# Kernel tuning notes

Hardware: AMD Instinct MI355X
Metric: run time of the kernel (lower is better)

## Reference

```python
import jax, jax.numpy as jnp
import numpy as np

B, S, HIDDEN, N_HEADS = 1, 2048, 2048, 16
HEAD_DIM = HIDDEN // N_HEADS  # 128


def setup_inputs() -> dict:
    key = jax.random.key(0)
    ks = jax.random.split(key, 7)
    w = 0.02  # init scale for projection weights
    return {
        "x_self": jax.random.normal(ks[0], (B, S, HIDDEN), jnp.float32),
        "x_cross": jax.random.normal(ks[1], (B, S, HIDDEN), jnp.float32),
        "mask": jnp.zeros((B, 1, S, S), jnp.float32),
        "Wq": jax.random.normal(ks[2], (HIDDEN, HIDDEN), jnp.float32) * w,
        "Wk": jax.random.normal(ks[3], (HIDDEN, HIDDEN), jnp.float32) * w,
        "Wv": jax.random.normal(ks[4], (HIDDEN, HIDDEN), jnp.float32) * w,
        "Wo": jax.random.normal(ks[5], (HIDDEN, HIDDEN), jnp.float32) * w,
    }


def reference(x_self, x_cross, mask, Wq, Wk, Wv, Wo):
    bf16 = jnp.bfloat16
    b = x_self.shape[0]
    scale = HEAD_DIM ** -0.5

    def split_heads(x):  # [b, s, hidden] -> [b, h, s, d]
        return x.reshape(b, -1, N_HEADS, HEAD_DIM).transpose(0, 2, 1, 3)

    # projections run in bf16 (weights cast to bf16 in the original)
    q_self = split_heads((x_self.astype(bf16) @ Wq.astype(bf16).T))
    q_cross = split_heads((x_cross.astype(bf16) @ Wq.astype(bf16).T))
    # k/v for both self and cross blocks come from x_self with identical weights
    k = split_heads((x_self.astype(bf16) @ Wk.astype(bf16).T))
    v = split_heads((x_self.astype(bf16) @ Wv.astype(bf16).T))

    def attn_block(qh):
        # fp32 upcast for QK^T + softmax, then bf16 cast for AV (dropout p=0 -> identity)
        w = jnp.einsum('bhqd,bhkd->bhqk', qh.astype(jnp.float32), k.astype(jnp.float32)) * scale
        w = w + mask
        w = jax.nn.softmax(w, axis=-1).astype(bf16)
        return jnp.einsum('bhqk,bhkd->bhqd', w, v.astype(bf16))  # [b, h, s, d] bf16

    out_self = attn_block(q_self)
    out_cross = attn_block(q_cross)
    out = jnp.concatenate([out_self, out_cross], axis=1)          # [b, 2h, s, d]
    out_flat = out.transpose(0, 2, 1, 3).reshape(b, -1, HIDDEN)   # [b, 2s, hidden]
    Wo_bf = Wo.astype(bf16)
    out_final = 0.5 * (out_flat @ Wo_bf.T + out_flat @ Wo_bf.T)
    return out_final.astype(jnp.float32)
```

## Files before the change

### kernel.cpp

```cpp
#include <hip/hip_runtime.h>
#include <hip/hip_bf16.h>
#include <stdint.h>

#define S 2048
#define HID 2048
#define NH 16
#define HD 128

typedef short short8 __attribute__((ext_vector_type(8)));
typedef float f32x4 __attribute__((ext_vector_type(4)));
typedef float f32x16 __attribute__((ext_vector_type(16)));
typedef uint32_t u32;
typedef u32 u32x4 __attribute__((ext_vector_type(4)));

__device__ __forceinline__ ushort f2bf(float x) {
  uint32_t u = __builtin_bit_cast(uint32_t, x);
  if ((u & 0x7fffffffu) > 0x7f800000u) return (ushort)((u >> 16) | 0x40);
  uint32_t r = u + 0x7fffu + ((u >> 16) & 1u);
  return (ushort)(r >> 16);
}
__device__ __forceinline__ float bf2f(ushort u) {
  union { uint32_t i; float f; } c; c.i = ((uint32_t)u) << 16; return c.f;
}

__device__ __forceinline__ void glds16(const ushort* g, ushort* l) {
  __builtin_amdgcn_global_load_lds((const __attribute__((address_space(1))) uint32_t*)g,
                                   (__attribute__((address_space(3))) uint32_t*)l, 16, 0, 0);
}

__device__ __forceinline__ void mfma16(f32x4& d, short8 a, short8 b) {
  asm volatile("v_mfma_f32_16x16x32_bf16 %0, %1, %2, %0" : "+v"(d) : "v"(a), "v"(b));
}
__device__ __forceinline__ void mfma32(f32x16& d, short8 a, short8 b) {
  asm volatile("v_mfma_f32_32x32x16_bf16 %0, %1, %2, %0" : "+v"(d) : "v"(a), "v"(b));
}
#define MFMA_FENCE() do {                              \
    asm volatile("s_nop 7\n\ts_nop 7\n\ts_nop 7");     \
    __builtin_amdgcn_sched_barrier(0);                 \
  } while (0)
__device__ __forceinline__ void plswap(u32& a, u32& b) {
  asm volatile("v_permlane32_swap_b32 %0, %1" : "+v"(a), "+v"(b));
}
__device__ __forceinline__ u32 cvtpk(float lo, float hi) {
  u32 r; asm volatile("v_cvt_pk_bf16_f32 %0, %1, %2" : "=v"(r) : "v"(lo), "v"(hi)); return r;
}

struct CastArgs { const float* s[6]; ushort* d[6]; };
__global__ __launch_bounds__(256) void cast6_k(CastArgs a) {
  const float* in = a.s[blockIdx.y];
  ushort* out = a.d[blockIdx.y];
  int i = blockIdx.x * 256 + threadIdx.x;
  float4 v = ((const float4*)in)[i];
  ushort4 o;
  o.x = f2bf(v.x); o.y = f2bf(v.y); o.z = f2bf(v.z); o.w = f2bf(v.w);
  ((ushort4*)out)[i] = o;
}

template <int OUTF32, int NSPLIT>
__global__ __launch_bounds__(256)
void gemm_bt_k(const ushort* __restrict__ A, const ushort* __restrict__ B,
               void* __restrict__ C, int M, int N, int K) {
  __shared__ __align__(16) ushort ldsA[128 * 64];
  __shared__ __align__(16) ushort ldsB[128 * 64];
  const int tid = threadIdx.x, lane = tid & 63, wid = tid >> 6;
  const int g = lane >> 4, c = lane & 15;
  const int wr = wid >> 1, wc = wid & 1;
  const long m0 = (long)blockIdx.y * 128, n0 = (long)blockIdx.x * 128;
  const int srow = lane >> 3, sslot = lane & 7;

  f32x4 acc[4][4] = {};

  for (int k0 = 0; k0 < K; k0 += 64) {
#pragma unroll
    for (int i = 0; i < 4; ++i) {
      int ii = wid * 4 + i;
      int rt = ii * 8 + srow;
      int col = ((sslot ^ (rt & 7)) << 3) + k0;
      glds16(A + (m0 + rt) * (long)K + col, ldsA + ii * 512);
      glds16(B + (n0 + rt) * (long)K + col, ldsB + ii * 512);
    }
    __syncthreads();
#pragma unroll
    for (int kk = 0; kk < 2; ++kk) {
      short8 af[4], bfr[4];
#pragma unroll
      for (int m = 0; m < 4; ++m) {
        int row = wr * 64 + m * 16 + c;
        af[m] = *(const short8*)(ldsA + row * 64 + (((kk * 4 + g) ^ (row & 7)) << 3));
      }
#pragma unroll
      for (int n = 0; n < 4; ++n) {
        int row = wc * 64 + n * 16 + c;
        bfr[n] = *(const short8*)(ldsB + row * 64 + (((kk * 4 + g) ^ (row & 7)) << 3));
      }
#pragma unroll
      for (int m = 0; m < 4; ++m)
#pragma unroll
        for (int n = 0; n < 4; ++n) mfma16(acc[m][n], af[m], bfr[n]);
    }
    __syncthreads();
  }
  MFMA_FENCE();
#pragma unroll
  for (int m = 0; m < 4; ++m) {
#pragma unroll
    for (int r = 0; r < 4; ++r) {
      long grow = m0 + wr * 64 + m * 16 + g * 4 + r;
#pragma unroll
      for (int n = 0; n < 4; ++n) {
        long gcol = n0 + wc * 64 + n * 16 + c;
        long idx;
        if (NSPLIT) idx = ((gcol >> 11) << 22) + (grow << 11) + (gcol & 2047);
        else        idx = grow * N + gcol;
        float v = acc[m][n][r];
        if (OUTF32) ((float*)C)[idx] = bf2f(f2bf(v));
        else        ((ushort*)C)[idx] = f2bf(v);
      }
    }
  }
}

__global__ __launch_bounds__(256)
void transpose_bf16_k(const ushort* __restrict__ in, ushort* __restrict__ out) {
  __shared__ __align__(16) ushort t[64][72];
  const int tid = threadIdx.x;
  const long bx = (long)blockIdx.x * 64;
  const long by = (long)blockIdx.y * 64;
#pragma unroll
  for (int i = 0; i < 2; ++i) {
    int row = (tid >> 3) + i * 32;
    int col = (tid & 7) * 8;
    *(short8*)(&t[row][col]) = *(const short8*)(in + (by + row) * 2048 + bx + col);
  }
  __syncthreads();
#pragma unroll
  for (int i = 0; i < 2; ++i) {
    int orow = (tid >> 3) + i * 32;
    int ocol = (tid & 7) * 8;
    short8 v;
#pragma unroll
    for (int j = 0; j < 8; ++j) v[j] = (short)t[ocol + j][orow];
    *(short8*)(out + (bx + orow) * 2048 + by + ocol) = v;
  }
}

__global__ __launch_bounds__(256)
void maskT_k(const float* __restrict__ in, ushort* __restrict__ out) {
  __shared__ ushort t[64][72];
  const int tid = threadIdx.x;
  const long q0 = (long)blockIdx.y * 64;
  const long k0 = (long)blockIdx.x * 64;
#pragma unroll
  for (int i = 0; i < 4; ++i) {
    int row = i * 16 + (tid >> 4);
    int col = (tid & 15) * 4;
    float4 v = *(const float4*)(in + (q0 + row) * S + k0 + col);
    t[col + 0][row] = f2bf(v.x);
    t[col + 1][row] = f2bf(v.y);
    t[col + 2][row] = f2bf(v.z);
    t[col + 3][row] = f2bf(v.w);
  }
  __syncthreads();
#pragma unroll
  for (int i = 0; i < 2; ++i) {
    int row = i * 32 + (tid >> 3);
    int col = (tid & 7) * 8;
    *(short8*)(out + (k0 + row) * S + q0 + col) = *(const short8*)(&t[row][col]);
  }
}

__global__ __launch_bounds__(256)
void attn4_k(const ushort* __restrict__ Qself, const ushort* __restrict__ Qcross,
             const ushort* __restrict__ Kp, const ushort* __restrict__ Vt,
             const ushort* __restrict__ maskT, ushort* __restrict__ outf) {
  __shared__ __align__(16) ushort ldsK[2 * 64 * 128];
  __shared__ __align__(16) ushort ldsV[2 * 128 * 64];
  const int tid = threadIdx.x, lane = tid & 63, wid = tid >> 6;
  const int c31 = lane & 31, hi = lane >> 5;

  const int b = blockIdx.x;
  const int xcd = b & 7, j = b >> 3;
  const int h = xcd + 8 * (j & 1);
  const int blk = (j >> 1) & 1;
  const int qt = j >> 2;

  const ushort* Qp = blk ? Qcross : Qself;
  const int qbase = qt * 128 + wid * 32;
  const long qme = qbase + c31;

  short8 qf[8];
#pragma unroll
  for (int ks = 0; ks < 8; ++ks)
    qf[ks] = *(const short8*)(Qp + qme * HID + h * HD + ks * 16 + hi * 8);

  f32x16 o[4] = {};
  float m_r = -__builtin_inff(), l_r = 0.f;

  const float SC  = 0.08838834764831845f;
  const float L2E = 1.4426950408889634f;
  const float THR = 5.545177444479562f;

  const int kRow4 = lane >> 4, kSlot = lane & 15;
  const int vRow8 = lane >> 3, vSlot = lane & 7;
  const ushort* mT = maskT + qme;

#define STAGE(BO, KV0) do {                                                       \
    _Pragma("unroll")                                                             \
    for (int i_ = 0; i_ < 4; ++i_) {                                              \
      int seg = i_ * 4 + wid;                                                     \
      int rk = seg * 4 + kRow4;                                                   \
      glds16(Kp + (long)((KV0) + rk) * HID + h * HD + ((kSlot ^ (rk & 15)) << 3), \
             ldsK + (BO) * 8192 + seg * 512);                                     \
      int rv = seg * 8 + vRow8;                                                   \
      glds16(Vt + (long)(h * HD + rv) * S + (KV0) + ((vSlot ^ (rv & 7)) << 3),    \
             ldsV + (BO) * 8192 + seg * 512);                                     \
    }                                                                             \
  } while (0)

  STAGE(0, 0);
  __syncthreads();

  for (int t = 0; t < 32; ++t) {
    const int bo = t & 1;
    const ushort* kb = ldsK + bo * 8192;
    const ushort* vb = ldsV + bo * 8192;
    if (t < 31) STAGE(bo ^ 1, (t + 1) * 64);
    const int kv0 = t * 64;

    ushort mvu0[16], mvu1[16];
#pragma unroll
    for (int r = 0; r < 16; ++r) {
      int krow = (r & 3) + 8 * (r >> 2) + 4 * hi;
      mvu0[r] = mT[(long)(kv0 + krow) * S];
      mvu1[r] = mT[(long)(kv0 + 32 + krow) * S];
    }

    f32x16 s0 = {}, s1 = {};
    __builtin_amdgcn_s_setprio(1);
#pragma unroll
    for (int ks = 0; ks < 8; ++ks) {
      int r0 = c31, r1 = 32 + c31;
      short8 kf0 = *(const short8*)(kb + r0 * 128 + (((ks * 2 + hi) ^ (r0 & 15)) << 3));
      short8 kf1 = *(const short8*)(kb + r1 * 128 + (((ks * 2 + hi) ^ (r1 & 15)) << 3));
      mfma32(s0, kf0, qf[ks]);
      mfma32(s1, kf1, qf[ks]);
    }
    __builtin_amdgcn_s_setprio(0);
    MFMA_FENCE();

#pragma unroll
    for (int r = 0; r < 16; ++r) {
      s0[r] = __builtin_fmaf(s0[r], SC, bf2f(mvu0[r]));
      s1[r] = __builtin_fmaf(s1[r], SC, bf2f(mvu1[r]));
    }

    float mx[16];
#pragma unroll
    for (int r = 0; r < 16; ++r) mx[r] = fmaxf(s0[r], s1[r]);
#pragma unroll
    for (int st = 8; st >= 1; st >>= 1)
#pragma unroll
      for (int i = 0; i < 8; ++i)
        if (i < st) mx[i] = fmaxf(mx[i], mx[i + st]);
    float pmax = fmaxf(mx[0], __shfl_xor(mx[0], 32));

    if (!__all(pmax <= m_r + THR)) {
      float mnew = fmaxf(m_r, pmax);
      float alpha = __builtin_amdgcn_exp2f((m_r - mnew) * L2E);
      m_r = mnew;
      l_r *= alpha;
#pragma unroll
      for (int r = 0; r < 16; ++r) {
        float alf = __shfl(alpha, (r & 3) + 8 * (r >> 2) + 4 * hi);
#pragma unroll
        for (int dt = 0; dt < 4; ++dt) o[dt][r] *= alf;
      }
    }

    const float nm = -m_r * L2E;
#pragma unroll
    for (int r = 0; r < 16; ++r) {
      s0[r] = __builtin_amdgcn_exp2f(__builtin_fmaf(s0[r], L2E, nm));
      s1[r] = __builtin_amdgcn_exp2f(__builtin_fmaf(s1[r], L2E, nm));
    }
    float sm[16];
#pragma unroll
    for (int r = 0; r < 16; ++r) sm[r] = s0[r] + s1[r];
#pragma unroll
    for (int st = 8; st >= 1; st >>= 1)
#pragma unroll
      for (int i = 0; i < 8; ++i)
        if (i < st) sm[i] += sm[i + st];
    l_r += sm[0] + __shfl_xor(sm[0], 32);

    short8 pa[4];
#pragma unroll
    for (int kk = 0; kk < 4; ++kk) {
      const f32x16& sv = (kk < 2) ? s0 : s1;
      const int bq = (kk & 1) * 8;
      u32 x0 = cvtpk(sv[bq + 0], sv[bq + 1]);
      u32 x1 = cvtpk(sv[bq + 2], sv[bq + 3]);
      u32 y0 = cvtpk(sv[bq + 4], sv[bq + 5]);
      u32 y1 = cvtpk(sv[bq + 6], sv[bq + 7]);
      plswap(x0, y0);
      plswap(x1, y1);
      u32x4 tt; tt[0] = x0; tt[1] = x1; tt[2] = y0; tt[3] = y1;
      pa[kk] = __builtin_bit_cast(short8, tt);
    }
    asm volatile("s_nop 1");
    __builtin_amdgcn_sched_barrier(0);

    __builtin_amdgcn_s_setprio(1);
#pragma unroll
    for (int dt = 0; dt < 4; ++dt) {
      int row = dt * 32 + c31;
#pragma unroll
      for (int kk = 0; kk < 4; ++kk) {
        short8 vf = *(const short8*)(vb + row * 64 + (((kk * 2 + hi) ^ (row & 7)) << 3));
        mfma32(o[dt], pa[kk], vf);
      }
    }
    __builtin_amdgcn_s_setprio(0);

    __syncthreads();
  }
#undef STAGE

  MFMA_FENCE();
#pragma unroll
  for (int r = 0; r < 16; ++r) {
    int qr = (r & 3) + 8 * (r >> 2) + 4 * hi;
    float linv = 1.0f / __shfl(l_r, qr);
    long orow = 2L * (qbase + qr) + blk;
#pragma unroll
    for (int dt = 0; dt < 4; ++dt)
      outf[orow * HID + h * HD + dt * 32 + c31] = f2bf(o[dt][r] * linv);
  }
}

extern "C" void kernel_launch(void* const* d_in, const int* in_sizes, int n_in,
                              void* d_out, int out_size, void* d_ws, size_t ws_size,
                              hipStream_t stream) {
  (void)in_sizes; (void)n_in; (void)out_size; (void)ws_size;
  const float* x_self  = (const float*)d_in[0];
  const float* x_cross = (const float*)d_in[1];
  const float* mask    = (const float*)d_in[2];
  const float* Wq      = (const float*)d_in[3];
  const float* Wk      = (const float*)d_in[4];
  const float* Wv      = (const float*)d_in[5];
  const float* Wo      = (const float*)d_in[6];

  uint8_t* w = (uint8_t*)d_ws;
  const size_t MB8 = (size_t)S * HID * sizeof(ushort);
  ushort* xs_bf   = (ushort*)(w + 0 * MB8);
  ushort* xc_bf   = (ushort*)(w + 1 * MB8);
  ushort* Wq_bf   = (ushort*)(w + 2 * MB8);
  ushort* Wk_bf   = (ushort*)(w + 3 * MB8);
  ushort* Wv_bf   = (ushort*)(w + 4 * MB8);
  ushort* Wo_bf   = (ushort*)(w + 5 * MB8);
  ushort* q_self  = (ushort*)(w + 6 * MB8);
  ushort* q_cross = (ushort*)(w + 7 * MB8);
  ushort* k_      = (ushort*)(w + 8 * MB8);
  ushort* v_      = (ushort*)(w + 9 * MB8);
  ushort* vt       = xs_bf;
  ushort* out_flat = Wq_bf;
  ushort* maskT    = v_;

  CastArgs ca;
  ca.s[0] = x_self;  ca.d[0] = xs_bf;
  ca.s[1] = x_cross; ca.d[1] = xc_bf;
  ca.s[2] = Wq;      ca.d[2] = Wq_bf;
  ca.s[3] = Wk;      ca.d[3] = Wk_bf;
  ca.s[4] = Wv;      ca.d[4] = Wv_bf;
  ca.s[5] = Wo;      ca.d[5] = Wo_bf;
  cast6_k<<<dim3(4096, 6), 256, 0, stream>>>(ca);

  gemm_bt_k<0, 0><<<dim3(16, 32), 256, 0, stream>>>(xs_bf, Wq_bf, q_self, 4096, 2048, 2048);
  gemm_bt_k<0, 1><<<dim3(32, 16), 256, 0, stream>>>(xs_bf, Wk_bf, k_, 2048, 4096, 2048);

  transpose_bf16_k<<<dim3(32, 32), 256, 0, stream>>>(v_, vt);
  maskT_k<<<dim3(32, 32), 256, 0, stream>>>(mask, maskT);

  attn4_k<<<dim3(512), 256, 0, stream>>>(q_self, q_cross, k_, vt, maskT, out_flat);

  gemm_bt_k<1, 0><<<dim3(16, 32), 256, 0, stream>>>(out_flat, Wo_bf, d_out, 4096, 2048, 2048);
}
```

Baseline: 253.4 us.

## Software-pipeline attention: overlap next tile's QK^T MFMAs with current softmax

The attention kernel now uses 32-row KV tiles in place of 64-row ones and restructures the loop so the QK^T MFMA cluster for tile t+1 is issued before the softmax and PV work for tile t. Two score accumulators ping-pong between iterations, and K is staged two tiles ahead while V is staged one tile ahead. The goal is to hide the exp/max/sum VALU work behind matrix-core work and to halve LDS use. The cost is twice as many iterations and barriers, and more live registers.

```diff
diff --git a/kernel.cpp b/kernel.cpp
--- a/kernel.cpp
+++ b/kernel.cpp
@@ -170,11 +170,11 @@
 }
 
 __global__ __launch_bounds__(256)
-void attn4_k(const ushort* __restrict__ Qself, const ushort* __restrict__ Qcross,
+void attn5_k(const ushort* __restrict__ Qself, const ushort* __restrict__ Qcross,
              const ushort* __restrict__ Kp, const ushort* __restrict__ Vt,
              const ushort* __restrict__ maskT, ushort* __restrict__ outf) {
-  __shared__ __align__(16) ushort ldsK[2 * 64 * 128];
-  __shared__ __align__(16) ushort ldsV[2 * 128 * 64];
+  __shared__ __align__(16) ushort ldsK[2 * 32 * 128];
+  __shared__ __align__(16) ushort ldsV[2 * 128 * 32];
   const int tid = threadIdx.x, lane = tid & 63, wid = tid >> 6;
   const int c31 = lane & 31, hi = lane >> 5;
 
@@ -194,137 +194,145 @@
     qf[ks] = *(const short8*)(Qp + qme * HID + h * HD + ks * 16 + hi * 8);
 
   f32x16 o[4] = {};
+  f32x16 sA, sB;
   float m_r = -__builtin_inff(), l_r = 0.f;
 
   const float SC  = 0.08838834764831845f;
   const float L2E = 1.4426950408889634f;
   const float THR = 5.545177444479562f;
 
-  const int kRow4 = lane >> 4, kSlot = lane & 15;
-  const int vRow8 = lane >> 3, vSlot = lane & 7;
+  const int kRow16 = lane >> 4, kSlot16 = lane & 15;
+  const int vRow4  = lane >> 2, vSlot4  = lane & 3;
   const ushort* mT = maskT + qme;
 
-#define STAGE(BO, KV0) do {                                                       \
-    _Pragma("unroll")                                                             \
-    for (int i_ = 0; i_ < 4; ++i_) {                                              \
-      int seg = i_ * 4 + wid;                                                     \
-      int rk = seg * 4 + kRow4;                                                   \
-      glds16(Kp + (long)((KV0) + rk) * HID + h * HD + ((kSlot ^ (rk & 15)) << 3), \
-             ldsK + (BO) * 8192 + seg * 512);                                     \
-      int rv = seg * 8 + vRow8;                                                   \
-      glds16(Vt + (long)(h * HD + rv) * S + (KV0) + ((vSlot ^ (rv & 7)) << 3),    \
-             ldsV + (BO) * 8192 + seg * 512);                                     \
-    }                                                                             \
+#define STAGE_K(BO, KV0) do {                                                      \
+    _Pragma("unroll")                                                              \
+    for (int i_ = 0; i_ < 2; ++i_) {                                               \
+      int seg = i_ * 4 + wid;                                                      \
+      int rk = seg * 4 + kRow16;                                                   \
+      glds16(Kp + (long)((KV0) + rk) * HID + h * HD + ((kSlot16 ^ (rk & 15)) << 3),\
+             ldsK + (BO) * 4096 + seg * 512);                                      \
+    } } while (0)
+
+#define STAGE_V(BO, KV0) do {                                                      \
+    _Pragma("unroll")                                                              \
+    for (int i_ = 0; i_ < 2; ++i_) {                                               \
+      int seg = i_ * 4 + wid;                                                      \
+      int rv = seg * 16 + vRow4;                                                   \
+      glds16(Vt + (long)(h * HD + rv) * S + (KV0) + ((vSlot4 ^ (rv & 3)) << 3),    \
+             ldsV + (BO) * 4096 + seg * 512);                                      \
+    } } while (0)
+
+#define QCLUSTER(SWR, KBASE) do {                                                  \
+    const ushort* kb_ = (KBASE);                                                   \
+    _Pragma("unroll")                                                              \
+    for (int r_ = 0; r_ < 16; ++r_) (SWR)[r_] = 0.f;                               \
+    __builtin_amdgcn_s_setprio(1);                                                 \
+    _Pragma("unroll")                                                              \
+    for (int ks = 0; ks < 8; ++ks) {                                               \
+      short8 kf = *(const short8*)(kb_ + c31 * 128 + (((ks * 2 + hi) ^ (c31 & 15)) << 3)); \
+      mfma32((SWR), kf, qf[ks]);                                                   \
+    }                                                                              \
+    __builtin_amdgcn_s_setprio(0);                                                 \
   } while (0)
 
-  STAGE(0, 0);
+#define BODY(T, SRD, SWR) do {                                                     \
+    const int kv0_ = (T) * 32;                                                     \
+    ushort mvu[16];                                                                \
+    _Pragma("unroll")                                                              \
+    for (int r = 0; r < 16; ++r) {                                                 \
+      int krow = (r & 3) + 8 * (r >> 2) + 4 * hi;                                  \
+      mvu[r] = mT[(long)(kv0_ + krow) * S];                                        \
+    }                                                                              \
+    if ((T) + 2 < 64) STAGE_K((T) & 1, ((T) + 2) * 32);                            \
+    if ((T) + 1 < 64) {                                                            \
+      STAGE_V(((T) + 1) & 1, ((T) + 1) * 32);                                      \
+      QCLUSTER(SWR, ldsK + (((T) + 1) & 1) * 4096);                                \
+    }                                                                              \
+    __builtin_amdgcn_sched_barrier(0);                                             \
+    _Pragma("unroll")                                                              \
+    for (int r = 0; r < 16; ++r)                                                   \
+      (SRD)[r] = __builtin_fmaf((SRD)[r], SC, bf2f(mvu[r]));                       \
+    float mx[8];                                                                   \
+    _Pragma("unroll")                                                              \
+    for (int i = 0; i < 8; ++i) mx[i] = fmaxf((SRD)[i], (SRD)[i + 8]);             \
+    _Pragma("unroll")                                                              \
+    for (int st = 4; st >= 1; st >>= 1)                                            \
+      _Pragma("unroll")                                                            \
+      for (int i = 0; i < 4; ++i)                                                  \
+        if (i < st) mx[i] = fmaxf(mx[i], mx[i + st]);                              \
+    float pmax = fmaxf(mx[0], __shfl_xor(mx[0], 32));                              \
+    if (!__all(pmax <= m_r + THR)) {                                               \
+      float mnew = fmaxf(m_r, pmax);                                               \
+      float alpha = __builtin_amdgcn_exp2f((m_r - mnew) * L2E);                    \
+      m_r = mnew; l_r *= alpha;                                                    \
+      _Pragma("unroll")                                                            \
+      for (int r = 0; r < 16; ++r) {                                               \
+        float alf = __shfl(alpha, (r & 3) + 8 * (r >> 2) + 4 * hi);                \
+        _Pragma("unroll")                                                          \
+        for (int dt = 0; dt < 4; ++dt) o[dt][r] *= alf;                            \
+      }                                                                            \
+    }                                                                              \
+    const float nm_ = -m_r * L2E;                                                  \
+    _Pragma("unroll")                                                              \
+    for (int r = 0; r < 16; ++r)                                                   \
+      (SRD)[r] = __builtin_amdgcn_exp2f(__builtin_fmaf((SRD)[r], L2E, nm_));       \
+    float sm[8];                                                                   \
+    _Pragma("unroll")                                                              \
+    for (int i = 0; i < 8; ++i) sm[i] = (SRD)[i] + (SRD)[i + 8];                   \
+    _Pragma("unroll")                                                              \
+    for (int st = 4; st >= 1; st >>= 1)                                            \
+      _Pragma("unroll")                                                            \
+      for (int i = 0; i < 4; ++i)                                                  \
+        if (i < st) sm[i] += sm[i + st];                                           \
+    l_r += sm[0] + __shfl_xor(sm[0], 32);                                          \
+    short8 pa[2];                                                                  \
+    _Pragma("unroll")                                                              \
+    for (int kk = 0; kk < 2; ++kk) {                                               \
+      const int bq = kk * 8;                                                       \
+      u32 x0 = cvtpk((SRD)[bq + 0], (SRD)[bq + 1]);                                \
+      u32 x1 = cvtpk((SRD)[bq + 2], (SRD)[bq + 3]);                                \
+      u32 y0 = cvtpk((SRD)[bq + 4], (SRD)[bq + 5]);                                \
+      u32 y1 = cvtpk((SRD)[bq + 6], (SRD)[bq + 7]);                                \
+      plswap(x0, y0);                                                              \
+      plswap(x1, y1);                                                              \
+      u32x4 tt; tt[0] = x0; tt[1] = x1; tt[2] = y0; tt[3] = y1;                    \
+      pa[kk] = __builtin_bit_cast(short8, tt);                                     \
+    }                                                                              \
+    asm volatile("s_nop 1");                                                       \
+    __builtin_amdgcn_sched_barrier(0);                                             \
+    {                                                                              \
+      const ushort* vb_ = ldsV + ((T) & 1) * 4096;                                 \
+      __builtin_amdgcn_s_setprio(1);                                               \
+      _Pragma("unroll")                                                            \
+      for (int dt = 0; dt < 4; ++dt) {                                             \
+        int row = dt * 32 + c31;                                                   \
+        _Pragma("unroll")                                                          \
+        for (int kk = 0; kk < 2; ++kk) {                                           \
+          short8 vf = *(const short8*)(vb_ + row * 32 + (((kk * 2 + hi) ^ (row & 3)) << 3)); \
+          mfma32(o[dt], pa[kk], vf);                                               \
+        }                                                                          \
+      }                                                                            \
+      __builtin_amdgcn_s_setprio(0);                                               \
+    }                                                                              \
+    __syncthreads();                                                               \
+  } while (0)
+
+  STAGE_K(0, 0);
+  STAGE_V(0, 0);
+  STAGE_K(1, 32);
   __syncthreads();
-
-  for (int t = 0; t < 32; ++t) {
-    const int bo = t & 1;
-    const ushort* kb = ldsK + bo * 8192;
-    const ushort* vb = ldsV + bo * 8192;
-    if (t < 31) STAGE(bo ^ 1, (t + 1) * 64);
-    const int kv0 = t * 64;
-
-    ushort mvu0[16], mvu1[16];
-#pragma unroll
-    for (int r = 0; r < 16; ++r) {
-      int krow = (r & 3) + 8 * (r >> 2) + 4 * hi;
-      mvu0[r] = mT[(long)(kv0 + krow) * S];
-      mvu1[r] = mT[(long)(kv0 + 32 + krow) * S];
-    }
-
-    f32x16 s0 = {}, s1 = {};
-    __builtin_amdgcn_s_setprio(1);
-#pragma unroll
-    for (int ks = 0; ks < 8; ++ks) {
-      int r0 = c31, r1 = 32 + c31;
-      short8 kf0 = *(const short8*)(kb + r0 * 128 + (((ks * 2 + hi) ^ (r0 & 15)) << 3));
-      short8 kf1 = *(const short8*)(kb + r1 * 128 + (((ks * 2 + hi) ^ (r1 & 15)) << 3));
-      mfma32(s0, kf0, qf[ks]);
-      mfma32(s1, kf1, qf[ks]);
-    }
-    __builtin_amdgcn_s_setprio(0);
-    MFMA_FENCE();
-
-#pragma unroll
-    for (int r = 0; r < 16; ++r) {
-      s0[r] = __builtin_fmaf(s0[r], SC, bf2f(mvu0[r]));
-      s1[r] = __builtin_fmaf(s1[r], SC, bf2f(mvu1[r]));
-    }
-
-    float mx[16];
-#pragma unroll
-    for (int r = 0; r < 16; ++r) mx[r] = fmaxf(s0[r], s1[r]);
-#pragma unroll
-    for (int st = 8; st >= 1; st >>= 1)
-#pragma unroll
-      for (int i = 0; i < 8; ++i)
-        if (i < st) mx[i] = fmaxf(mx[i], mx[i + st]);
-    float pmax = fmaxf(mx[0], __shfl_xor(mx[0], 32));
-
-    if (!__all(pmax <= m_r + THR)) {
-      float mnew = fmaxf(m_r, pmax);
-      float alpha = __builtin_amdgcn_exp2f((m_r - mnew) * L2E);
-      m_r = mnew;
-      l_r *= alpha;
-#pragma unroll
-      for (int r = 0; r < 16; ++r) {
-        float alf = __shfl(alpha, (r & 3) + 8 * (r >> 2) + 4 * hi);
-#pragma unroll
-        for (int dt = 0; dt < 4; ++dt) o[dt][r] *= alf;
-      }
-    }
-
-    const float nm = -m_r * L2E;
-#pragma unroll
-    for (int r = 0; r < 16; ++r) {
-      s0[r] = __builtin_amdgcn_exp2f(__builtin_fmaf(s0[r], L2E, nm));
-      s1[r] = __builtin_amdgcn_exp2f(__builtin_fmaf(s1[r], L2E, nm));
-    }
-    float sm[16];
-#pragma unroll
-    for (int r = 0; r < 16; ++r) sm[r] = s0[r] + s1[r];
-#pragma unroll
-    for (int st = 8; st >= 1; st >>= 1)
-#pragma unroll
-      for (int i = 0; i < 8; ++i)
-        if (i < st) sm[i] += sm[i + st];
-    l_r += sm[0] + __shfl_xor(sm[0], 32);
-
-    short8 pa[4];
-#pragma unroll
-    for (int kk = 0; kk < 4; ++kk) {
-      const f32x16& sv = (kk < 2) ? s0 : s1;
-      const int bq = (kk & 1) * 8;
-      u32 x0 = cvtpk(sv[bq + 0], sv[bq + 1]);
-      u32 x1 = cvtpk(sv[bq + 2], sv[bq + 3]);
-      u32 y0 = cvtpk(sv[bq + 4], sv[bq + 5]);
-      u32 y1 = cvtpk(sv[bq + 6], sv[bq + 7]);
-      plswap(x0, y0);
-      plswap(x1, y1);
-      u32x4 tt; tt[0] = x0; tt[1] = x1; tt[2] = y0; tt[3] = y1;
-      pa[kk] = __builtin_bit_cast(short8, tt);
-    }
-    asm volatile("s_nop 1");
-    __builtin_amdgcn_sched_barrier(0);
-
-    __builtin_amdgcn_s_setprio(1);
-#pragma unroll
-    for (int dt = 0; dt < 4; ++dt) {
-      int row = dt * 32 + c31;
-#pragma unroll
-      for (int kk = 0; kk < 4; ++kk) {
-        short8 vf = *(const short8*)(vb + row * 64 + (((kk * 2 + hi) ^ (row & 7)) << 3));
-        mfma32(o[dt], pa[kk], vf);
-      }
-    }
-    __builtin_amdgcn_s_setprio(0);
-
-    __syncthreads();
-  }
-#undef STAGE
+  QCLUSTER(sA, ldsK);
+  MFMA_FENCE();
+
+  for (int t = 0; t < 64; t += 2) {
+    BODY(t, sA, sB);
+    BODY(t + 1, sB, sA);
+  }
+#undef BODY
+#undef QCLUSTER
+#undef STAGE_V
+#undef STAGE_K
 
   MFMA_FENCE();
 #pragma unroll
@@ -381,7 +389,7 @@
   transpose_bf16_k<<<dim3(32, 32), 256, 0, stream>>>(v_, vt);
   maskT_k<<<dim3(32, 32), 256, 0, stream>>>(mask, maskT);
 
-  attn4_k<<<dim3(512), 256, 0, stream>>>(q_self, q_cross, k_, vt, maskT, out_flat);
+  attn5_k<<<dim3(512), 256, 0, stream>>>(q_self, q_cross, k_, vt, maskT, out_flat);
 
   gemm_bt_k<1, 0><<<dim3(16, 32), 256, 0, stream>>>(out_flat, Wo_bf, d_out, 4096, 2048, 2048);
 }
```

Result: no change. 257.1 us (+1.5%).

## Double-buffer GEMM LDS tiles and use raw barriers with partial vmcnt waits

Applied to the files above, without the earlier changes.

The GEMM kernel gains double-buffered LDS staging. The next K tile is issued before computing the current one, and a partial s_waitcnt vmcnt plus a raw s_barrier replace the full __syncthreads drains. The attention kernel likewise issues the next K/V stage after the mask loads and waits only on the older loads via vmcnt(40). Both aim to overlap global-to-LDS traffic with MFMA work and avoid full memory drains at barriers. This relies on hand-counted vmcnt values, adds redundant wraparound loads on the last iteration, and doubles GEMM LDS use, which may lower occupancy.

```diff
diff --git a/kernel.cpp b/kernel.cpp
--- a/kernel.cpp
+++ b/kernel.cpp
@@ -38,6 +38,8 @@
     asm volatile("s_nop 7\n\ts_nop 7\n\ts_nop 7");     \
     __builtin_amdgcn_sched_barrier(0);                 \
   } while (0)
+#define RAW_BARRIER() asm volatile("s_barrier" ::: "memory")
+#define SCHED_FENCE() __builtin_amdgcn_sched_barrier(0)
 __device__ __forceinline__ void plswap(u32& a, u32& b) {
   asm volatile("v_permlane32_swap_b32 %0, %1" : "+v"(a), "+v"(b));
 }
@@ -60,8 +62,8 @@
 __global__ __launch_bounds__(256)
 void gemm_bt_k(const ushort* __restrict__ A, const ushort* __restrict__ B,
                void* __restrict__ C, int M, int N, int K) {
-  __shared__ __align__(16) ushort ldsA[128 * 64];
-  __shared__ __align__(16) ushort ldsB[128 * 64];
+  __shared__ __align__(16) ushort ldsA[2 * 128 * 64];
+  __shared__ __align__(16) ushort ldsB[2 * 128 * 64];
   const int tid = threadIdx.x, lane = tid & 63, wid = tid >> 6;
   const int g = lane >> 4, c = lane & 15;
   const int wr = wid >> 1, wc = wid & 1;
@@ -70,36 +72,49 @@
 
   f32x4 acc[4][4] = {};
 
+#define GSTAGE(BO, K0) do {                                                \
+    _Pragma("unroll")                                                      \
+    for (int i_ = 0; i_ < 4; ++i_) {                                       \
+      int ii = wid * 4 + i_;                                               \
+      int rt = ii * 8 + srow;                                              \
+      int col = ((sslot ^ (rt & 7)) << 3) + (K0);                          \
+      glds16(A + (m0 + rt) * (long)K + col, ldsA + (BO) * 8192 + ii * 512);\
+      glds16(B + (n0 + rt) * (long)K + col, ldsB + (BO) * 8192 + ii * 512);\
+    } } while (0)
+
+  GSTAGE(0, 0);
+
+#pragma clang loop unroll(disable)
   for (int k0 = 0; k0 < K; k0 += 64) {
-#pragma unroll
-    for (int i = 0; i < 4; ++i) {
-      int ii = wid * 4 + i;
-      int rt = ii * 8 + srow;
-      int col = ((sslot ^ (rt & 7)) << 3) + k0;
-      glds16(A + (m0 + rt) * (long)K + col, ldsA + ii * 512);
-      glds16(B + (n0 + rt) * (long)K + col, ldsB + ii * 512);
-    }
-    __syncthreads();
+    const int bo = (k0 >> 6) & 1;
+    GSTAGE(bo ^ 1, (k0 + 64 < K) ? (k0 + 64) : 0);
+    SCHED_FENCE();
+    asm volatile("s_waitcnt vmcnt(8)");
+    SCHED_FENCE();
+    RAW_BARRIER();
+    const ushort* la = ldsA + bo * 8192;
+    const ushort* lb = ldsB + bo * 8192;
 #pragma unroll
     for (int kk = 0; kk < 2; ++kk) {
       short8 af[4], bfr[4];
 #pragma unroll
       for (int m = 0; m < 4; ++m) {
         int row = wr * 64 + m * 16 + c;
-        af[m] = *(const short8*)(ldsA + row * 64 + (((kk * 4 + g) ^ (row & 7)) << 3));
+        af[m] = *(const short8*)(la + row * 64 + (((kk * 4 + g) ^ (row & 7)) << 3));
       }
 #pragma unroll
       for (int n = 0; n < 4; ++n) {
         int row = wc * 64 + n * 16 + c;
-        bfr[n] = *(const short8*)(ldsB + row * 64 + (((kk * 4 + g) ^ (row & 7)) << 3));
+        bfr[n] = *(const short8*)(lb + row * 64 + (((kk * 4 + g) ^ (row & 7)) << 3));
       }
 #pragma unroll
       for (int m = 0; m < 4; ++m)
 #pragma unroll
         for (int n = 0; n < 4; ++n) mfma16(acc[m][n], af[m], bfr[n]);
     }
-    __syncthreads();
-  }
+    RAW_BARRIER();
+  }
+#undef GSTAGE
   MFMA_FENCE();
 #pragma unroll
   for (int m = 0; m < 4; ++m) {
@@ -170,7 +185,7 @@
 }
 
 __global__ __launch_bounds__(256)
-void attn4_k(const ushort* __restrict__ Qself, const ushort* __restrict__ Qcross,
+void attn6_k(const ushort* __restrict__ Qself, const ushort* __restrict__ Qcross,
              const ushort* __restrict__ Kp, const ushort* __restrict__ Vt,
              const ushort* __restrict__ maskT, ushort* __restrict__ outf) {
   __shared__ __align__(16) ushort ldsK[2 * 64 * 128];
@@ -218,13 +233,12 @@
   } while (0)
 
   STAGE(0, 0);
-  __syncthreads();
-
+
+#pragma clang loop unroll(disable)
   for (int t = 0; t < 32; ++t) {
     const int bo = t & 1;
     const ushort* kb = ldsK + bo * 8192;
     const ushort* vb = ldsV + bo * 8192;
-    if (t < 31) STAGE(bo ^ 1, (t + 1) * 64);
     const int kv0 = t * 64;
 
     ushort mvu0[16], mvu1[16];
@@ -234,6 +248,12 @@
       mvu0[r] = mT[(long)(kv0 + krow) * S];
       mvu1[r] = mT[(long)(kv0 + 32 + krow) * S];
     }
+    SCHED_FENCE();
+    STAGE(bo ^ 1, ((t + 1) & 31) * 64);
+    SCHED_FENCE();
+    asm volatile("s_waitcnt vmcnt(40)");
+    SCHED_FENCE();
+    RAW_BARRIER();
 
     f32x16 s0 = {}, s1 = {};
     __builtin_amdgcn_s_setprio(1);
@@ -308,7 +328,7 @@
       pa[kk] = __builtin_bit_cast(short8, tt);
     }
     asm volatile("s_nop 1");
-    __builtin_amdgcn_sched_barrier(0);
+    SCHED_FENCE();
 
     __builtin_amdgcn_s_setprio(1);
 #pragma unroll
@@ -322,7 +342,7 @@
     }
     __builtin_amdgcn_s_setprio(0);
 
-    __syncthreads();
+    RAW_BARRIER();
   }
 #undef STAGE
 
@@ -381,7 +401,7 @@
   transpose_bf16_k<<<dim3(32, 32), 256, 0, stream>>>(v_, vt);
   maskT_k<<<dim3(32, 32), 256, 0, stream>>>(mask, maskT);
 
-  attn4_k<<<dim3(512), 256, 0, stream>>>(q_self, q_cross, k_, vt, maskT, out_flat);
+  attn6_k<<<dim3(512), 256, 0, stream>>>(q_self, q_cross, k_, vt, maskT, out_flat);
 
   gemm_bt_k<1, 0><<<dim3(16, 32), 256, 0, stream>>>(out_flat, Wo_bf, d_out, 4096, 2048, 2048);
 }
```

Measured after the change: 260.2 us. 1.03x slower.

## Repack mask into 4-key groups and restructure attention loop barriers

Applied to the files above, without the earlier changes.

The mask is now stored in a layout that interleaves groups of four key rows per query, so each lane fetches its mask values with eight 8-byte loads instead of thirty-two scalar 2-byte loads. The attention loop issues mask and next-tile K/V loads up front, waits with a partial vmcnt and raw s_barrier instead of __syncthreads, and wraps the prefetch index so it always stages. The row-max reduction now uses three-input max trees, and the PV loop order is swapped so consecutive MFMAs go to different accumulators. The hand-tuned waitcnt and barrier placement depend on exact load counts and risk subtle races if the count is wrong. The final iteration also issues a redundant prefetch.

```diff
diff --git a/kernel.cpp b/kernel.cpp
--- a/kernel.cpp
+++ b/kernel.cpp
@@ -38,6 +38,9 @@
     asm volatile("s_nop 7\n\ts_nop 7\n\ts_nop 7");     \
     __builtin_amdgcn_sched_barrier(0);                 \
   } while (0)
+#define RAW_BARRIER() asm volatile("s_barrier" ::: "memory")
+#define SCHED_FENCE() __builtin_amdgcn_sched_barrier(0)
+#define MAX3(a, b, c) fmaxf(fmaxf((a), (b)), (c))
 __device__ __forceinline__ void plswap(u32& a, u32& b) {
   asm volatile("v_permlane32_swap_b32 %0, %1" : "+v"(a), "+v"(b));
 }
@@ -145,7 +148,7 @@
 }
 
 __global__ __launch_bounds__(256)
-void maskT_k(const float* __restrict__ in, ushort* __restrict__ out) {
+void maskQ_k(const float* __restrict__ in, ushort* __restrict__ out) {
   __shared__ ushort t[64][72];
   const int tid = threadIdx.x;
   const long q0 = (long)blockIdx.y * 64;
@@ -162,17 +165,22 @@
   }
   __syncthreads();
 #pragma unroll
-  for (int i = 0; i < 2; ++i) {
-    int row = i * 32 + (tid >> 3);
-    int col = (tid & 7) * 8;
-    *(short8*)(out + (k0 + row) * S + q0 + col) = *(const short8*)(&t[row][col]);
+  for (int i = 0; i < 4; ++i) {
+    int r4 = i * 4 + (tid >> 6);
+    int q = tid & 63;
+    ushort4 o;
+    o.x = t[r4 * 4 + 0][q];
+    o.y = t[r4 * 4 + 1][q];
+    o.z = t[r4 * 4 + 2][q];
+    o.w = t[r4 * 4 + 3][q];
+    *(ushort4*)(out + ((k0 >> 2) + r4) * (S * 4) + (q0 + q) * 4) = o;
   }
 }
 
 __global__ __launch_bounds__(256)
-void attn4_k(const ushort* __restrict__ Qself, const ushort* __restrict__ Qcross,
+void attn7_k(const ushort* __restrict__ Qself, const ushort* __restrict__ Qcross,
              const ushort* __restrict__ Kp, const ushort* __restrict__ Vt,
-             const ushort* __restrict__ maskT, ushort* __restrict__ outf) {
+             const ushort* __restrict__ maskQ, ushort* __restrict__ outf) {
   __shared__ __align__(16) ushort ldsK[2 * 64 * 128];
   __shared__ __align__(16) ushort ldsV[2 * 128 * 64];
   const int tid = threadIdx.x, lane = tid & 63, wid = tid >> 6;
@@ -202,7 +210,7 @@
 
   const int kRow4 = lane >> 4, kSlot = lane & 15;
   const int vRow8 = lane >> 3, vSlot = lane & 7;
-  const ushort* mT = maskT + qme;
+  const ushort* mqp = maskQ + qme * 4 + hi * (S * 4);
 
 #define STAGE(BO, KV0) do {                                                       \
     _Pragma("unroll")                                                             \
@@ -218,22 +226,23 @@
   } while (0)
 
   STAGE(0, 0);
-  __syncthreads();
-
+
+#pragma clang loop unroll(disable)
   for (int t = 0; t < 32; ++t) {
     const int bo = t & 1;
     const ushort* kb = ldsK + bo * 8192;
     const ushort* vb = ldsV + bo * 8192;
-    if (t < 31) STAGE(bo ^ 1, (t + 1) * 64);
-    const int kv0 = t * 64;
-
-    ushort mvu0[16], mvu1[16];
-#pragma unroll
-    for (int r = 0; r < 16; ++r) {
-      int krow = (r & 3) + 8 * (r >> 2) + 4 * hi;
-      mvu0[r] = mT[(long)(kv0 + krow) * S];
-      mvu1[r] = mT[(long)(kv0 + 32 + krow) * S];
-    }
+
+    ushort4 mq4[8];
+#pragma unroll
+    for (int jj = 0; jj < 8; ++jj)
+      mq4[jj] = *(const ushort4*)(mqp + ((jj & 3) * 2 + (jj >> 2) * 8) * (S * 4));
+    SCHED_FENCE();
+    STAGE(bo ^ 1, ((t + 1) & 31) * 64);
+    SCHED_FENCE();
+    asm volatile("s_waitcnt vmcnt(16)");
+    SCHED_FENCE();
+    RAW_BARRIER();
 
     f32x16 s0 = {}, s1 = {};
     __builtin_amdgcn_s_setprio(1);
@@ -250,19 +259,27 @@
 
 #pragma unroll
     for (int r = 0; r < 16; ++r) {
-      s0[r] = __builtin_fmaf(s0[r], SC, bf2f(mvu0[r]));
-      s1[r] = __builtin_fmaf(s1[r], SC, bf2f(mvu1[r]));
-    }
-
-    float mx[16];
-#pragma unroll
-    for (int r = 0; r < 16; ++r) mx[r] = fmaxf(s0[r], s1[r]);
-#pragma unroll
-    for (int st = 8; st >= 1; st >>= 1)
-#pragma unroll
-      for (int i = 0; i < 8; ++i)
-        if (i < st) mx[i] = fmaxf(mx[i], mx[i + st]);
-    float pmax = fmaxf(mx[0], __shfl_xor(mx[0], 32));
+      s0[r] = __builtin_fmaf(s0[r], SC, bf2f(mq4[r >> 2][r & 3]));
+      s1[r] = __builtin_fmaf(s1[r], SC, bf2f(mq4[4 + (r >> 2)][r & 3]));
+    }
+
+    float a0 = MAX3(s0[0], s0[1], s0[2]);
+    float a1 = MAX3(s0[3], s0[4], s0[5]);
+    float a2 = MAX3(s0[6], s0[7], s0[8]);
+    float a3 = MAX3(s0[9], s0[10], s0[11]);
+    float a4 = MAX3(s0[12], s0[13], s0[14]);
+    float a5 = MAX3(s0[15], s1[0], s1[1]);
+    float a6 = MAX3(s1[2], s1[3], s1[4]);
+    float a7 = MAX3(s1[5], s1[6], s1[7]);
+    float a8 = MAX3(s1[8], s1[9], s1[10]);
+    float a9 = MAX3(s1[11], s1[12], s1[13]);
+    float a10 = fmaxf(s1[14], s1[15]);
+    float b0 = MAX3(a0, a1, a2);
+    float b1 = MAX3(a3, a4, a5);
+    float b2 = MAX3(a6, a7, a8);
+    float b3 = fmaxf(a9, a10);
+    float pm = MAX3(b0, b1, fmaxf(b2, b3));
+    float pmax = fmaxf(pm, __shfl_xor(pm, 32));
 
     if (!__all(pmax <= m_r + THR)) {
       float mnew = fmaxf(m_r, pmax);
@@ -308,21 +325,22 @@
       pa[kk] = __builtin_bit_cast(short8, tt);
     }
     asm volatile("s_nop 1");
-    __builtin_amdgcn_sched_barrier(0);
+    SCHED_FENCE();
 
     __builtin_amdgcn_s_setprio(1);
 #pragma unroll
-    for (int dt = 0; dt < 4; ++dt) {
-      int row = dt * 32 + c31;
-#pragma unroll
-      for (int kk = 0; kk < 4; ++kk) {
+    for (int kk = 0; kk < 4; ++kk) {
+#pragma unroll
+      for (int dt = 0; dt < 4; ++dt) {
+        int row = dt * 32 + c31;
         short8 vf = *(const short8*)(vb + row * 64 + (((kk * 2 + hi) ^ (row & 7)) << 3));
         mfma32(o[dt], pa[kk], vf);
       }
     }
     __builtin_amdgcn_s_setprio(0);
 
-    __syncthreads();
+    RAW_BARRIER();
+    mqp += 16 * (S * 4);
   }
 #undef STAGE
 
@@ -364,7 +382,7 @@
   ushort* v_      = (ushort*)(w + 9 * MB8);
   ushort* vt       = xs_bf;
   ushort* out_flat = Wq_bf;
-  ushort* maskT    = v_;
+  ushort* maskQ    = v_;
 
   CastArgs ca;
   ca.s[0] = x_self;  ca.d[0] = xs_bf;
@@ -379,9 +397,9 @@
   gemm_bt_k<0, 1><<<dim3(32, 16), 256, 0, stream>>>(xs_bf, Wk_bf, k_, 2048, 4096, 2048);
 
   transpose_bf16_k<<<dim3(32, 32), 256, 0, stream>>>(v_, vt);
-  maskT_k<<<dim3(32, 32), 256, 0, stream>>>(mask, maskT);
-
-  attn4_k<<<dim3(512), 256, 0, stream>>>(q_self, q_cross, k_, vt, maskT, out_flat);
+  maskQ_k<<<dim3(32, 32), 256, 0, stream>>>(mask, maskQ);
+
+  attn7_k<<<dim3(512), 256, 0, stream>>>(q_self, q_cross, k_, vt, maskQ, out_flat);
 
   gemm_bt_k<1, 0><<<dim3(16, 32), 256, 0, stream>>>(out_flat, Wo_bf, d_out, 4096, 2048, 2048);
 }
```

Result: faster. 245.8 us (-3.0%).
